# Performance work log

Measured on AMD Instinct MI355X. Metric: run time of the kernel, lower is better.

Reference implementation:

```python
import jax, jax.numpy as jnp
import numpy as np

B, S, D = 2, 2048, 1024
H, DK, DV = 16, 64, 64

def setup_inputs() -> dict:
    key = jax.random.key(0)
    ks = jax.random.split(key, 16)
    sc = 0.02
    inp = {
        'Q': jax.random.normal(ks[0], (B, S, D), jnp.float32),
        'K': jax.random.normal(ks[1], (B, S, D), jnp.float32),
        'V': jax.random.normal(ks[2], (B, S, D), jnp.float32),
        'attn_mask': jax.random.randint(ks[3], (B, S, S), 0, 2) > 0,
        'wq': jax.random.normal(ks[4], (H * DK, D), jnp.float32) * sc,
        'bq': jnp.zeros((H * DK,), jnp.float32),
        'wk': jax.random.normal(ks[5], (H * DK, D), jnp.float32) * sc,
        'bk': jnp.zeros((H * DK,), jnp.float32),
        'wv': jax.random.normal(ks[6], (H * DV, D), jnp.float32) * sc,
        'bv': jnp.zeros((H * DV,), jnp.float32),
        'wo': jax.random.normal(ks[7], (D, H * DV), jnp.float32) * sc,
        'bo': jnp.zeros((D,), jnp.float32),
        'gamma': jnp.ones((D,), jnp.float32),
        'beta': jnp.zeros((D,), jnp.float32),
    }
    return inp

def reference(Q, K, V, attn_mask, wq, bq, wk, bk, wv, bv, wo, bo, gamma, beta):
    b = Q.shape[0]
    # Faithful to torch: .view(B, H, -1, dk) with NO transpose (reshape-based head split)
    q = (Q @ wq.T + bq).reshape(b, H, -1, DK)
    k = (K @ wk.T + bk).reshape(b, H, -1, DK)
    v = (V @ wv.T + bv).reshape(b, H, -1, DV)
    scores = jnp.einsum('bhqd,bhkd->bhqk', q, k) / np.sqrt(DK).astype(np.float32)
    scores = jnp.where(attn_mask[:, None, :, :], jnp.float32(-1e9), scores)
    attn = jax.nn.softmax(scores, axis=-1)
    context = jnp.einsum('bhqk,bhkd->bhqd', attn, v)  # [B,H,S,dv]
    context = context.transpose(0, 2, 1, 3).reshape(b, -1, H * DV)
    output = context @ wo.T + bo
    x = output + Q
    mu = jnp.mean(x, axis=-1, keepdims=True)
    var = jnp.var(x, axis=-1, keepdims=True)
    return (x - mu) / jnp.sqrt(var + 1e-5) * gamma + beta
```

## Files before the change

### kernel.cpp

```cpp
#include <hip/hip_runtime.h>
#include <hip/hip_bf16.h>
#include <stdint.h>

typedef __bf16 bf16_t;
typedef __bf16 bf16x8 __attribute__((ext_vector_type(8)));
typedef __bf16 bf16x4 __attribute__((ext_vector_type(4)));
typedef float  f32x4  __attribute__((ext_vector_type(4)));

#if __has_builtin(__builtin_amdgcn_exp2f)
#define EXP2F __builtin_amdgcn_exp2f
#else
#define EXP2F exp2f
#endif


__device__ __forceinline__ void async_copy16(void* lds, const void* gptr) {
  __builtin_amdgcn_global_load_lds(
      (const __attribute__((address_space(1))) void*)gptr,
      (__attribute__((address_space(3))) void*)lds, 16, 0, 0);
}

__device__ __forceinline__ f32x4 splat4(float x) {
  f32x4 r; r[0] = x; r[1] = x; r[2] = x; r[3] = x; return r;
}

__device__ __forceinline__ bool detect_fp32(const void* p) {
  const uint16_t* h = (const uint16_t*)p;
  int weird_even = 0, zero_even = 0, nz_odd = 0;
  for (int i = 0; i < 32; ++i) {
    uint16_t e = h[2 * i], o = h[2 * i + 1];
    int ee = (e >> 7) & 0xFF;
    if (e == 0) zero_even++;
    else if (ee < 90 || ee > 160) weird_even++;
    if (o != 0) nz_odd++;
  }
  return (weird_even >= 6) || (zero_even == 32 && nz_odd >= 1);
}

__global__ __launch_bounds__(256) void convert_all(
    const void* s0, const void* s1, const void* s2, const void* s3,
    const void* s4, const void* s5, const void* s6, const void* s7,
    const void* s8, const void* s9, const void* s10, const void* s11,
    const void* s12, char* __restrict__ ws) {
  const void* srcs[13] = {s0, s1, s2, s3, s4, s5, s6, s7, s8, s9, s10, s11, s12};
  const int counts[13] = {4194304, 4194304, 4194304,
                          1048576, 1024, 1048576, 1024,
                          1048576, 1024, 1048576, 1024,
                          1024, 1024};
  const size_t dofs[13] = {
      0ull, 8ull << 20, 16ull << 20,
      24ull << 20, (32ull << 20) + 0 * 8192, 26ull << 20, (32ull << 20) + 1 * 8192,
      28ull << 20, (32ull << 20) + 2 * 8192, 30ull << 20, (32ull << 20) + 3 * 8192,
      (32ull << 20) + 4 * 8192, (32ull << 20) + 5 * 8192};
  const int bi = blockIdx.y;
  const void* src = srcs[bi];
  bf16x8* dst = (bf16x8*)(ws + dofs[bi]);
  const int nv = counts[bi] >> 3;
  const bool f32 = detect_fp32(src);
  const int idx = blockIdx.x * 256 + threadIdx.x;
  const int stride = gridDim.x * 256;
  if (f32) {
    const float4* s4p = (const float4*)src;
    for (int i = idx; i < nv; i += stride) {
      float4 a = s4p[2 * i], b = s4p[2 * i + 1];
      bf16x8 o;
      o[0] = (bf16_t)a.x; o[1] = (bf16_t)a.y; o[2] = (bf16_t)a.z; o[3] = (bf16_t)a.w;
      o[4] = (bf16_t)b.x; o[5] = (bf16_t)b.y; o[6] = (bf16_t)b.z; o[7] = (bf16_t)b.w;
      dst[i] = o;
    }
  } else {
    const bf16x8* s8p = (const bf16x8*)src;
    for (int i = idx; i < nv; i += stride) dst[i] = s8p[i];
  }
}

__device__ __forceinline__ int detect_mask(const uint8_t* p) {
  const uint32_t* w = (const uint32_t*)p;
  bool i32 = true;
  for (int i = 0; i < 32; ++i) i32 &= (w[i] <= 1u);
  if (i32) return 0;
  const uint16_t* hh = (const uint16_t*)p;
  bool evz = true, oddok = true, allbf = true, allf16 = true;
  for (int i = 0; i < 32; ++i) {
    uint16_t e = hh[2 * i], o = hh[2 * i + 1];
    evz &= (e == 0);
    oddok &= (o == 0 || o == 0x3F80);
    allbf &= (e == 0 || e == 0x3F80) && (o == 0 || o == 0x3F80);
    allf16 &= (e == 0 || e == 0x3C00) && (o == 0 || o == 0x3C00);
  }
  if (evz && oddok) return 1;
  if (allbf || allf16) return 2;
  return 3;
}

__global__ __launch_bounds__(256) void mask_pack(const uint8_t* __restrict__ mraw,
                                                 uint8_t* __restrict__ outp) {
  const int mode = detect_mask(mraw);
  const int bq = blockIdx.x;
  const int L = threadIdx.x;
  uint32_t byte = 0;
  if (mode <= 1) {
    const uint4* m = (const uint4*)mraw;
    const size_t b4 = (size_t)bq * 512 + L * 2;
    uint4 a = m[b4], c = m[b4 + 1];
    byte = (a.x != 0u ? 1u : 0u) | (a.y != 0u ? 2u : 0u) |
           (a.z != 0u ? 4u : 0u) | (a.w != 0u ? 8u : 0u) |
           (c.x != 0u ? 16u : 0u) | (c.y != 0u ? 32u : 0u) |
           (c.z != 0u ? 64u : 0u) | (c.w != 0u ? 128u : 0u);
  } else if (mode == 2) {
    const uint16_t* m = (const uint16_t*)mraw;
    const size_t base = (size_t)bq * 2048 + L * 8;
    for (int j = 0; j < 8; ++j) byte |= (m[base + j] != 0 ? 1u : 0u) << j;
  } else {
    const size_t base = (size_t)bq * 2048 + L * 8;
    for (int j = 0; j < 8; ++j) byte |= (mraw[base + j] != 0 ? 1u : 0u) << j;
  }
  outp[(size_t)bq * 256 + L] = (uint8_t)byte;
}

template <int MODE>
__device__ __forceinline__ void gemm_tile(const bf16_t* __restrict__ X,
                                          const bf16_t* __restrict__ W,
                                          const bf16_t* __restrict__ bias,
                                          const bf16_t* __restrict__ QresB,
                                          const float* __restrict__ QresF,
                                          bool qres_is_f32,
                                          void* __restrict__ outv) {
  __shared__ __align__(16) bf16_t sA[128 * 32];
  __shared__ __align__(16) bf16_t sB[128 * 32];
  const int tm = blockIdx.x * 128;
  const int tn = blockIdx.y * 128;
  const int t = threadIdx.x;
  const int w = t >> 6, l = t & 63, lc = l & 15, ql = l >> 4;
  const int wm = (w >> 1) * 64, wn = (w & 1) * 64;
  f32x4 acc[4][4];
  for (int i = 0; i < 4; ++i)
    for (int j = 0; j < 4; ++j) acc[i][j] = splat4(0.0f);

  const int m0 = t >> 2;
  const int kc0 = (t & 3) * 8;

  for (int k0 = 0; k0 < 1024; k0 += 32) {
    __syncthreads();
    async_copy16((char*)sA + w * 1024,        X + (size_t)(tm + m0) * 1024 + k0 + kc0);
    async_copy16((char*)sA + 4096 + w * 1024, X + (size_t)(tm + 64 + m0) * 1024 + k0 + kc0);
    async_copy16((char*)sB + w * 1024,        W + (size_t)(tn + m0) * 1024 + k0 + kc0);
    async_copy16((char*)sB + 4096 + w * 1024, W + (size_t)(tn + 64 + m0) * 1024 + k0 + kc0);
    __syncthreads();

    bf16x8 af[4], bfr[4];
    for (int i = 0; i < 4; ++i)
      af[i] = *(const bf16x8*)(sA + (wm + i * 16 + lc) * 32 + ql * 8);
    for (int j = 0; j < 4; ++j)
      bfr[j] = *(const bf16x8*)(sB + (wn + j * 16 + lc) * 32 + ql * 8);
    for (int i = 0; i < 4; ++i)
      for (int j = 0; j < 4; ++j)
        acc[i][j] = __builtin_amdgcn_mfma_f32_16x16x32_bf16(af[i], bfr[j], acc[i][j], 0, 0, 0);
  }

  float bvals[4];
  for (int j = 0; j < 4; ++j) bvals[j] = (float)bias[tn + wn + j * 16 + lc];
  for (int i = 0; i < 4; ++i) {
    for (int j = 0; j < 4; ++j) {
      const int col = tn + wn + j * 16 + lc;
      for (int v = 0; v < 4; ++v) {
        const int row = tm + wm + i * 16 + ql * 4 + v;
        float val = acc[i][j][v] + bvals[j];
        if (MODE == 0) {
          ((bf16_t*)outv)[(size_t)row * 1024 + col] = (bf16_t)val;
        } else if (MODE == 3) {
          ((bf16_t*)outv)[(size_t)row * 1024 + col] = (bf16_t)(val * 0.18033688f);
        } else if (MODE == 1) {
          const int b = row >> 11;
          const int x = (row & 2047) * 1024 + col;
          const int h = x >> 17;
          const int s = (x >> 6) & 2047;
          const int d = x & 63;
          ((bf16_t*)outv)[(size_t)((b * 16 + h) * 64 + d) * 2048 + s] = (bf16_t)val;
        } else {
          val += qres_is_f32 ? QresF[(size_t)row * 1024 + col]
                             : (float)QresB[(size_t)row * 1024 + col];
          ((float*)outv)[(size_t)row * 1024 + col] = val;
        }
      }
    }
  }
}

__global__ __launch_bounds__(256, 2) void qkv_gemm(
    const bf16_t* __restrict__ Q, const bf16_t* __restrict__ K, const bf16_t* __restrict__ V,
    const bf16_t* __restrict__ wq, const bf16_t* __restrict__ bq,
    const bf16_t* __restrict__ wk, const bf16_t* __restrict__ bk,
    const bf16_t* __restrict__ wv, const bf16_t* __restrict__ bv,
    bf16_t* __restrict__ qlin, bf16_t* __restrict__ klin, bf16_t* __restrict__ vT) {
  if (blockIdx.z == 0)      gemm_tile<3>(Q, wq, bq, nullptr, nullptr, false, qlin);
  else if (blockIdx.z == 1) gemm_tile<0>(K, wk, bk, nullptr, nullptr, false, klin);
  else                      gemm_tile<1>(V, wv, bv, nullptr, nullptr, false, vT);
}

__global__ __launch_bounds__(256, 2) void final_gemm(
    const bf16_t* __restrict__ ctx, const bf16_t* __restrict__ wo,
    const bf16_t* __restrict__ bo, const bf16_t* __restrict__ QresB,
    const void* __restrict__ Qraw, float* __restrict__ xres) {
  const bool qf32 = detect_fp32(Qraw);
  gemm_tile<2>(ctx, wo, bo, QresB, (const float*)Qraw, qf32, xres);
}

__global__ __launch_bounds__(512, 4) void attn(const bf16_t* __restrict__ qlin,
                                               const bf16_t* __restrict__ klin,
                                               const bf16_t* __restrict__ vT,
                                               const uint8_t* __restrict__ mQb,
                                               bf16_t* __restrict__ ctx) {
  __shared__ __align__(16) bf16_t sK[128 * 64];
  __shared__ __align__(16) bf16_t sVt[64 * 128];
  __shared__ __align__(16) uint8_t sM[128 * 16];

  const int t = threadIdx.x, w = t >> 6, l = t & 63, lc = l & 15, ql = l >> 4;
  const int bid = blockIdx.x;
  const int qt = bid & 15, h = (bid >> 4) & 15, b = bid >> 8;
  const int q0 = qt * 128, rb = w * 16;

  const bf16_t* qh = qlin + (size_t)(b * 16 + h) * 2048 * 64;
  const bf16_t* kh = klin + (size_t)(b * 16 + h) * 2048 * 64;
  const bf16_t* vh = vT   + (size_t)(b * 16 + h) * 64 * 2048;
  const uint8_t* mh = mQb + ((size_t)(b * 2048 + q0)) * 256;

  const int kRow = t >> 3;
  const int kChk = (t & 7) ^ ((t >> 3) & 7);
  const int vRow = t >> 4;
  const int vChk = (t & 15) ^ ((t >> 4) & 15);

  bf16x8 qf[2];
  for (int c = 0; c < 2; ++c)
    qf[c] = *(const bf16x8*)(qh + (size_t)(q0 + rb + lc) * 64 + c * 32 + ql * 8);

  float l_st = 0.0f;
  f32x4 oacc[4];
  for (int n = 0; n < 4; ++n) oacc[n] = splat4(0.0f);

  for (int kt = 0; kt < 16; ++kt) {
    const int k0 = kt * 128;
    __syncthreads();
    for (int is = 0; is < 2; ++is)
      async_copy16((char*)sK + is * 8192 + w * 1024,
                   kh + (size_t)(k0 + is * 64 + kRow) * 64 + kChk * 8);
    for (int is = 0; is < 2; ++is)
      async_copy16((char*)sVt + is * 8192 + w * 1024,
                   vh + (size_t)(is * 32 + vRow) * 2048 + k0 + vChk * 8);
    if (w < 2)
      async_copy16((char*)sM + w * 1024, mh + (size_t)(w * 64 + l) * 256 + kt * 16);
    __syncthreads();

    f32x4 sc[8];
    for (int j = 0; j < 8; ++j) {
      const char* kbase = (const char*)sK + (j * 16 + lc) * 128;
      bf16x8 ka0 = *(const bf16x8*)(kbase + ((ql    ) ^ (lc & 7)) * 16);
      bf16x8 ka1 = *(const bf16x8*)(kbase + ((ql + 4) ^ (lc & 7)) * 16);
      sc[j] = __builtin_amdgcn_mfma_f32_16x16x32_bf16(ka0, qf[0], splat4(0.0f), 0, 0, 0);
      sc[j] = __builtin_amdgcn_mfma_f32_16x16x32_bf16(ka1, qf[1], sc[j], 0, 0, 0);
    }

    const uint4 mq = *(const uint4*)(sM + (rb + lc) * 16);
    const uint32_t mwarr[4] = {mq.x, mq.y, mq.z, mq.w};
    bf16x4 pa[8];
    float rsum = 0.0f;
    for (int j = 0; j < 8; ++j) {
      const uint32_t m4 = mwarr[j >> 1] >> (((j & 1) << 4) + (ql << 2));
      bf16x4 pj;
      for (int v = 0; v < 4; ++v) {
        float e = EXP2F(fminf(sc[j][v], 80.0f));
        e = ((m4 >> v) & 1u) ? 0.0f : e;
        rsum += e;
        pj[v] = (bf16_t)e;
      }
      pa[j] = pj;
    }
    rsum += __shfl_xor(rsum, 16, 64);
    rsum += __shfl_xor(rsum, 32, 64);
    l_st += rsum;

    for (int p = 0; p < 4; ++p) {
      bf16x8 a0;
      for (int v = 0; v < 4; ++v) { a0[v] = pa[2 * p][v]; a0[4 + v] = pa[2 * p + 1][v]; }
      for (int n = 0; n < 4; ++n) {
        const char* vrow = (const char*)sVt + (n * 16 + lc) * 256 + (ql & 1) * 8;
        const bf16x4 v0 = *(const bf16x4*)(vrow + (((4 * p     + (ql >> 1)) ^ lc) * 16));
        const bf16x4 v1 = *(const bf16x4*)(vrow + (((4 * p + 2 + (ql >> 1)) ^ lc) * 16));
        bf16x8 vb;
        for (int v = 0; v < 4; ++v) { vb[v] = v0[v]; vb[4 + v] = v1[v]; }
        oacc[n] = __builtin_amdgcn_mfma_f32_16x16x32_bf16(a0, vb, oacc[n], 0, 0, 0);
      }
    }
  }

  f32x4 linv;
  for (int v = 0; v < 4; ++v) linv[v] = 1.0f / __shfl(l_st, ql * 20 + v, 64);
  for (int n = 0; n < 4; ++n) {
    f32x4 o = oacc[n] * linv;
    for (int v = 0; v < 4; ++v) {
      const int row = q0 + rb + ql * 4 + v;
      ctx[(size_t)(b * 2048 + row) * 1024 + h * 64 + n * 16 + lc] = (bf16_t)o[v];
    }
  }
}

__global__ __launch_bounds__(256) void ln_k(float* __restrict__ x,
                                            const bf16_t* __restrict__ gamma,
                                            const bf16_t* __restrict__ beta) {
  const int row = blockIdx.x, t = threadIdx.x, w = t >> 6, l = t & 63;
  float* xr = x + (size_t)row * 1024;
  float4 xv = ((const float4*)xr)[t];
  float v0 = xv.x, v1 = xv.y, v2 = xv.z, v3 = xv.w;
  float s1 = v0 + v1 + v2 + v3;
  float s2 = v0 * v0 + v1 * v1 + v2 * v2 + v3 * v3;
  for (int d = 1; d < 64; d <<= 1) {
    s1 += __shfl_xor(s1, d, 64);
    s2 += __shfl_xor(s2, d, 64);
  }
  __shared__ float red[8];
  if (l == 0) { red[w] = s1; red[4 + w] = s2; }
  __syncthreads();
  s1 = red[0] + red[1] + red[2] + red[3];
  s2 = red[4] + red[5] + red[6] + red[7];
  const float mean = s1 * (1.0f / 1024.0f);
  const float var = s2 * (1.0f / 1024.0f) - mean * mean;
  const float rstd = rsqrtf(var + 1e-5f);
  bf16x4 gv = *(const bf16x4*)(gamma + t * 4);
  bf16x4 bv = *(const bf16x4*)(beta + t * 4);
  float4 ov;
  ov.x = (v0 - mean) * rstd * (float)gv[0] + (float)bv[0];
  ov.y = (v1 - mean) * rstd * (float)gv[1] + (float)bv[1];
  ov.z = (v2 - mean) * rstd * (float)gv[2] + (float)bv[2];
  ov.w = (v3 - mean) * rstd * (float)gv[3] + (float)bv[3];
  ((float4*)xr)[t] = ov;
}

extern "C" void kernel_launch(void* const* d_in, const int* in_sizes, int n_in,
                              void* d_out, int out_size, void* d_ws, size_t ws_size,
                              hipStream_t stream) {
  const uint8_t* msk = (const uint8_t*)d_in[3];

  char* ws = (char*)d_ws;
  bf16_t* Qc   = (bf16_t*)(ws + 0);
  bf16_t* Kc   = (bf16_t*)(ws + (8ull << 20));
  bf16_t* Vc   = (bf16_t*)(ws + (16ull << 20));
  bf16_t* wqc  = (bf16_t*)(ws + (24ull << 20));
  bf16_t* wkc  = (bf16_t*)(ws + (26ull << 20));
  bf16_t* wvc  = (bf16_t*)(ws + (28ull << 20));
  bf16_t* woc  = (bf16_t*)(ws + (30ull << 20));
  bf16_t* bqc  = (bf16_t*)(ws + (32ull << 20) + 0 * 8192);
  bf16_t* bkc  = (bf16_t*)(ws + (32ull << 20) + 1 * 8192);
  bf16_t* bvc  = (bf16_t*)(ws + (32ull << 20) + 2 * 8192);
  bf16_t* boc  = (bf16_t*)(ws + (32ull << 20) + 3 * 8192);
  bf16_t* gc   = (bf16_t*)(ws + (32ull << 20) + 4 * 8192);
  bf16_t* bec  = (bf16_t*)(ws + (32ull << 20) + 5 * 8192);
  uint8_t* mQb = (uint8_t*)(ws + (33ull << 20));
  bf16_t* qlin = (bf16_t*)(ws + (34ull << 20));
  bf16_t* klin = (bf16_t*)(ws + (42ull << 20));
  bf16_t* vT   = (bf16_t*)(ws + (50ull << 20));
  bf16_t* ctx  = Kc;
  float* outF  = (float*)d_out;

  convert_all<<<dim3(512, 13), 256, 0, stream>>>(
      d_in[0], d_in[1], d_in[2], d_in[4], d_in[5], d_in[6], d_in[7],
      d_in[8], d_in[9], d_in[10], d_in[11], d_in[12], d_in[13], ws);
  mask_pack<<<dim3(4096), 256, 0, stream>>>(msk, mQb);
  qkv_gemm<<<dim3(32, 8, 3), 256, 0, stream>>>(Qc, Kc, Vc, wqc, bqc, wkc, bkc,
                                               wvc, bvc, qlin, klin, vT);
  attn<<<dim3(512), 512, 0, stream>>>(qlin, klin, vT, mQb, ctx);
  final_gemm<<<dim3(32, 8), 256, 0, stream>>>(ctx, woc, boc, Qc, d_in[0], outF);
  ln_k<<<dim3(4096), 256, 0, stream>>>(outF, gc, bec);
}
```

Before: 328.0 us.

## Enlarge attention key tiles, MFMA row sums, and halve output-GEMM M tile

The attention kernel now stages 256 keys per iteration and processes them in two 128-key halves, which halves the number of barrier-separated load rounds. The softmax row sum is no longer built with per-lane VALU adds and cross-lane shuffles; it is accumulated by an extra MFMA against a vector of bf16 ones, so the sum uses the same bf16-rounded probabilities as the PV product. The final projection GEMM gains a 64-row tile variant, which doubles its grid and should spread work better across CUs. In exchange, attention LDS roughly doubles per block, which lowers how many blocks fit per CU. The bf16 residual pointer is replaced by nullptr, leaving only the fp32 Q path safe.

```diff
diff --git a/kernel.cpp b/kernel.cpp
--- a/kernel.cpp
+++ b/kernel.cpp
@@ -118,50 +118,54 @@
   outp[(size_t)bq * 256 + L] = (uint8_t)byte;
 }
 
-template <int MODE>
+template <int MODE, int BM>
 __device__ __forceinline__ void gemm_tile(const bf16_t* __restrict__ X,
                                           const bf16_t* __restrict__ W,
                                           const bf16_t* __restrict__ bias,
+                                          const float* __restrict__ QresF,
                                           const bf16_t* __restrict__ QresB,
-                                          const float* __restrict__ QresF,
                                           bool qres_is_f32,
                                           void* __restrict__ outv) {
-  __shared__ __align__(16) bf16_t sA[128 * 32];
+  __shared__ __align__(16) bf16_t sA[BM * 32];
   __shared__ __align__(16) bf16_t sB[128 * 32];
-  const int tm = blockIdx.x * 128;
+  const int tm = blockIdx.x * BM;
   const int tn = blockIdx.y * 128;
   const int t = threadIdx.x;
   const int w = t >> 6, l = t & 63, lc = l & 15, ql = l >> 4;
-  const int wm = (w >> 1) * 64, wn = (w & 1) * 64;
-  f32x4 acc[4][4];
+  const int wm = (BM == 128) ? (w >> 1) * 64 : 0;
+  const int wn = (BM == 128) ? (w & 1) * 64 : w * 32;
+  const int NJ = (BM == 128) ? 4 : 2;
+  f32x4 acc[4][(BM == 128) ? 4 : 2];
   for (int i = 0; i < 4; ++i)
-    for (int j = 0; j < 4; ++j) acc[i][j] = splat4(0.0f);
+    for (int j = 0; j < NJ; ++j) acc[i][j] = splat4(0.0f);
 
   const int m0 = t >> 2;
   const int kc0 = (t & 3) * 8;
 
   for (int k0 = 0; k0 < 1024; k0 += 32) {
     __syncthreads();
-    async_copy16((char*)sA + w * 1024,        X + (size_t)(tm + m0) * 1024 + k0 + kc0);
-    async_copy16((char*)sA + 4096 + w * 1024, X + (size_t)(tm + 64 + m0) * 1024 + k0 + kc0);
+    async_copy16((char*)sA + w * 1024, X + (size_t)(tm + m0) * 1024 + k0 + kc0);
+    if (BM == 128)
+      async_copy16((char*)sA + 4096 + w * 1024,
+                   X + (size_t)(tm + 64 + m0) * 1024 + k0 + kc0);
     async_copy16((char*)sB + w * 1024,        W + (size_t)(tn + m0) * 1024 + k0 + kc0);
     async_copy16((char*)sB + 4096 + w * 1024, W + (size_t)(tn + 64 + m0) * 1024 + k0 + kc0);
     __syncthreads();
 
-    bf16x8 af[4], bfr[4];
+    bf16x8 af[4], bfr[(BM == 128) ? 4 : 2];
     for (int i = 0; i < 4; ++i)
       af[i] = *(const bf16x8*)(sA + (wm + i * 16 + lc) * 32 + ql * 8);
-    for (int j = 0; j < 4; ++j)
+    for (int j = 0; j < NJ; ++j)
       bfr[j] = *(const bf16x8*)(sB + (wn + j * 16 + lc) * 32 + ql * 8);
     for (int i = 0; i < 4; ++i)
-      for (int j = 0; j < 4; ++j)
+      for (int j = 0; j < NJ; ++j)
         acc[i][j] = __builtin_amdgcn_mfma_f32_16x16x32_bf16(af[i], bfr[j], acc[i][j], 0, 0, 0);
   }
 
-  float bvals[4];
-  for (int j = 0; j < 4; ++j) bvals[j] = (float)bias[tn + wn + j * 16 + lc];
+  float bvals[(BM == 128) ? 4 : 2];
+  for (int j = 0; j < NJ; ++j) bvals[j] = (float)bias[tn + wn + j * 16 + lc];
   for (int i = 0; i < 4; ++i) {
-    for (int j = 0; j < 4; ++j) {
+    for (int j = 0; j < NJ; ++j) {
       const int col = tn + wn + j * 16 + lc;
       for (int v = 0; v < 4; ++v) {
         const int row = tm + wm + i * 16 + ql * 4 + v;
@@ -193,9 +197,9 @@
     const bf16_t* __restrict__ wk, const bf16_t* __restrict__ bk,
     const bf16_t* __restrict__ wv, const bf16_t* __restrict__ bv,
     bf16_t* __restrict__ qlin, bf16_t* __restrict__ klin, bf16_t* __restrict__ vT) {
-  if (blockIdx.z == 0)      gemm_tile<3>(Q, wq, bq, nullptr, nullptr, false, qlin);
-  else if (blockIdx.z == 1) gemm_tile<0>(K, wk, bk, nullptr, nullptr, false, klin);
-  else                      gemm_tile<1>(V, wv, bv, nullptr, nullptr, false, vT);
+  if (blockIdx.z == 0)      gemm_tile<3, 128>(Q, wq, bq, nullptr, nullptr, false, qlin);
+  else if (blockIdx.z == 1) gemm_tile<0, 128>(K, wk, bk, nullptr, nullptr, false, klin);
+  else                      gemm_tile<1, 128>(V, wv, bv, nullptr, nullptr, false, vT);
 }
 
 __global__ __launch_bounds__(256, 2) void final_gemm(
@@ -203,7 +207,7 @@
     const bf16_t* __restrict__ bo, const bf16_t* __restrict__ QresB,
     const void* __restrict__ Qraw, float* __restrict__ xres) {
   const bool qf32 = detect_fp32(Qraw);
-  gemm_tile<2>(ctx, wo, bo, QresB, (const float*)Qraw, qf32, xres);
+  gemm_tile<2, 64>(ctx, wo, bo, (const float*)Qraw, QresB, qf32, xres);
 }
 
 __global__ __launch_bounds__(512, 4) void attn(const bf16_t* __restrict__ qlin,
@@ -211,9 +215,9 @@
                                                const bf16_t* __restrict__ vT,
                                                const uint8_t* __restrict__ mQb,
                                                bf16_t* __restrict__ ctx) {
-  __shared__ __align__(16) bf16_t sK[128 * 64];
-  __shared__ __align__(16) bf16_t sVt[64 * 128];
-  __shared__ __align__(16) uint8_t sM[128 * 16];
+  __shared__ __align__(16) bf16_t sK[256 * 64];
+  __shared__ __align__(16) bf16_t sVt[64 * 256];
+  __shared__ __align__(16) uint8_t sM[128 * 32];
 
   const int t = threadIdx.x, w = t >> 6, l = t & 63, lc = l & 15, ql = l >> 4;
   const int bid = blockIdx.x;
@@ -227,74 +231,76 @@
 
   const int kRow = t >> 3;
   const int kChk = (t & 7) ^ ((t >> 3) & 7);
-  const int vRow = t >> 4;
-  const int vChk = (t & 15) ^ ((t >> 4) & 15);
+  const int vRow = t >> 5;
+  const int vChk = (t & 31) ^ ((t >> 5) & 15);
 
   bf16x8 qf[2];
   for (int c = 0; c < 2; ++c)
     qf[c] = *(const bf16x8*)(qh + (size_t)(q0 + rb + lc) * 64 + c * 32 + ql * 8);
 
-  float l_st = 0.0f;
-  f32x4 oacc[4];
+  bf16x8 vones;
+  for (int v = 0; v < 8; ++v) vones[v] = (bf16_t)1.0f;
+
+  f32x4 oacc[4], osum = splat4(0.0f);
   for (int n = 0; n < 4; ++n) oacc[n] = splat4(0.0f);
 
-  for (int kt = 0; kt < 16; ++kt) {
-    const int k0 = kt * 128;
+  for (int kt = 0; kt < 8; ++kt) {
+    const int k0 = kt * 256;
     __syncthreads();
-    for (int is = 0; is < 2; ++is)
+    for (int is = 0; is < 4; ++is)
       async_copy16((char*)sK + is * 8192 + w * 1024,
                    kh + (size_t)(k0 + is * 64 + kRow) * 64 + kChk * 8);
-    for (int is = 0; is < 2; ++is)
+    for (int is = 0; is < 4; ++is)
       async_copy16((char*)sVt + is * 8192 + w * 1024,
-                   vh + (size_t)(is * 32 + vRow) * 2048 + k0 + vChk * 8);
-    if (w < 2)
-      async_copy16((char*)sM + w * 1024, mh + (size_t)(w * 64 + l) * 256 + kt * 16);
+                   vh + (size_t)(is * 16 + vRow) * 2048 + k0 + vChk * 8);
+    if (w < 4)
+      async_copy16((char*)sM + w * 1024,
+                   mh + (size_t)(w * 32 + (l >> 1)) * 256 + kt * 32 + (l & 1) * 16);
     __syncthreads();
 
-    f32x4 sc[8];
-    for (int j = 0; j < 8; ++j) {
-      const char* kbase = (const char*)sK + (j * 16 + lc) * 128;
-      bf16x8 ka0 = *(const bf16x8*)(kbase + ((ql    ) ^ (lc & 7)) * 16);
-      bf16x8 ka1 = *(const bf16x8*)(kbase + ((ql + 4) ^ (lc & 7)) * 16);
-      sc[j] = __builtin_amdgcn_mfma_f32_16x16x32_bf16(ka0, qf[0], splat4(0.0f), 0, 0, 0);
-      sc[j] = __builtin_amdgcn_mfma_f32_16x16x32_bf16(ka1, qf[1], sc[j], 0, 0, 0);
-    }
-
-    const uint4 mq = *(const uint4*)(sM + (rb + lc) * 16);
-    const uint32_t mwarr[4] = {mq.x, mq.y, mq.z, mq.w};
-    bf16x4 pa[8];
-    float rsum = 0.0f;
-    for (int j = 0; j < 8; ++j) {
-      const uint32_t m4 = mwarr[j >> 1] >> (((j & 1) << 4) + (ql << 2));
-      bf16x4 pj;
-      for (int v = 0; v < 4; ++v) {
-        float e = EXP2F(fminf(sc[j][v], 80.0f));
-        e = ((m4 >> v) & 1u) ? 0.0f : e;
-        rsum += e;
-        pj[v] = (bf16_t)e;
+    for (int hf = 0; hf < 2; ++hf) {
+      f32x4 sc[8];
+      for (int j = 0; j < 8; ++j) {
+        const char* kbase = (const char*)sK + (hf * 128 + j * 16 + lc) * 128;
+        bf16x8 ka0 = *(const bf16x8*)(kbase + ((ql    ) ^ (lc & 7)) * 16);
+        bf16x8 ka1 = *(const bf16x8*)(kbase + ((ql + 4) ^ (lc & 7)) * 16);
+        sc[j] = __builtin_amdgcn_mfma_f32_16x16x32_bf16(ka0, qf[0], splat4(0.0f), 0, 0, 0);
+        sc[j] = __builtin_amdgcn_mfma_f32_16x16x32_bf16(ka1, qf[1], sc[j], 0, 0, 0);
       }
-      pa[j] = pj;
-    }
-    rsum += __shfl_xor(rsum, 16, 64);
-    rsum += __shfl_xor(rsum, 32, 64);
-    l_st += rsum;
-
-    for (int p = 0; p < 4; ++p) {
-      bf16x8 a0;
-      for (int v = 0; v < 4; ++v) { a0[v] = pa[2 * p][v]; a0[4 + v] = pa[2 * p + 1][v]; }
-      for (int n = 0; n < 4; ++n) {
-        const char* vrow = (const char*)sVt + (n * 16 + lc) * 256 + (ql & 1) * 8;
-        const bf16x4 v0 = *(const bf16x4*)(vrow + (((4 * p     + (ql >> 1)) ^ lc) * 16));
-        const bf16x4 v1 = *(const bf16x4*)(vrow + (((4 * p + 2 + (ql >> 1)) ^ lc) * 16));
-        bf16x8 vb;
-        for (int v = 0; v < 4; ++v) { vb[v] = v0[v]; vb[4 + v] = v1[v]; }
-        oacc[n] = __builtin_amdgcn_mfma_f32_16x16x32_bf16(a0, vb, oacc[n], 0, 0, 0);
+
+      const uint4 mq = *(const uint4*)(sM + (rb + lc) * 32 + hf * 16);
+      const uint32_t mwarr[4] = {mq.x, mq.y, mq.z, mq.w};
+      bf16x4 pa[8];
+      for (int j = 0; j < 8; ++j) {
+        const uint32_t m4 = mwarr[j >> 1] >> (((j & 1) << 4) + (ql << 2));
+        bf16x4 pj;
+        for (int v = 0; v < 4; ++v) {
+          float e = EXP2F(fminf(sc[j][v], 80.0f));
+          pj[v] = ((m4 >> v) & 1u) ? (bf16_t)0.0f : (bf16_t)e;
+        }
+        pa[j] = pj;
+      }
+
+      for (int p = 0; p < 4; ++p) {
+        bf16x8 a0;
+        for (int v = 0; v < 4; ++v) { a0[v] = pa[2 * p][v]; a0[4 + v] = pa[2 * p + 1][v]; }
+        osum = __builtin_amdgcn_mfma_f32_16x16x32_bf16(a0, vones, osum, 0, 0, 0);
+        for (int n = 0; n < 4; ++n) {
+          const char* vrow = (const char*)sVt + (n * 16 + lc) * 512 + (ql & 1) * 8;
+          const int c0 = (hf * 16 + 4 * p     + (ql >> 1)) ^ lc;
+          const int c1 = (hf * 16 + 4 * p + 2 + (ql >> 1)) ^ lc;
+          const bf16x4 v0 = *(const bf16x4*)(vrow + c0 * 16);
+          const bf16x4 v1 = *(const bf16x4*)(vrow + c1 * 16);
+          bf16x8 vb;
+          for (int v = 0; v < 4; ++v) { vb[v] = v0[v]; vb[4 + v] = v1[v]; }
+          oacc[n] = __builtin_amdgcn_mfma_f32_16x16x32_bf16(a0, vb, oacc[n], 0, 0, 0);
+        }
       }
     }
   }
 
   f32x4 linv;
-  for (int v = 0; v < 4; ++v) linv[v] = 1.0f / __shfl(l_st, ql * 20 + v, 64);
+  for (int v = 0; v < 4; ++v) linv[v] = 1.0f / osum[v];
   for (int n = 0; n < 4; ++n) {
     f32x4 o = oacc[n] * linv;
     for (int v = 0; v < 4; ++v) {
@@ -368,6 +374,6 @@
   qkv_gemm<<<dim3(32, 8, 3), 256, 0, stream>>>(Qc, Kc, Vc, wqc, bqc, wkc, bkc,
                                                wvc, bvc, qlin, klin, vT);
   attn<<<dim3(512), 512, 0, stream>>>(qlin, klin, vT, mQb, ctx);
-  final_gemm<<<dim3(32, 8), 256, 0, stream>>>(ctx, woc, boc, Qc, d_in[0], outF);
+  final_gemm<<<dim3(64, 8), 256, 0, stream>>>(ctx, woc, boc, nullptr, d_in[0], outF);
   ln_k<<<dim3(4096), 256, 0, stream>>>(outF, gc, bec);
 }
```

Result: faster. 317.4 us (-3.2%).
